# Performance work log

Measured on AMD Instinct MI355X. Metric: run time of the kernel, lower is better.

The kernel has to match this reference:

```python
import jax, jax.numpy as jnp
import numpy as np

N, E, D, L, R = 100000, 500000, 128, 2, 10
EPS = 1e-5  # BatchNorm1d default eps


def setup_inputs() -> dict:
    key = jax.random.key(0)
    ks = jax.random.split(key, 10)
    return {
        "in_node_emb": jax.random.normal(ks[0], (N, D), jnp.float32),
        "in_rel_emb": jax.random.normal(ks[1], (R, D), jnp.float32),
        "w_in": jax.random.normal(ks[2], (L, D, D), jnp.float32) * 0.05,
        "w_out": jax.random.normal(ks[3], (L, D, D), jnp.float32) * 0.05,
        "w_loop": jax.random.normal(ks[4], (L, D, D), jnp.float32) * 0.05,
        "w_rel": jax.random.normal(ks[5], (L, D, D), jnp.float32) * 0.05,
        "loop_rel": jax.random.normal(ks[6], (L, 1, D), jnp.float32) * 0.05,
        "bias": jnp.zeros((L, D), jnp.float32),
        "edge_src": jax.random.randint(ks[7], (E,), 0, N),
        "edge_dst": jax.random.randint(ks[8], (E,), 0, N),
        "edge_type": jax.random.randint(ks[9], (E,), 0, R),
    }


def _gcn_forward(in_node_emb, in_rel_emb, w_in, w_out, w_loop, w_rel, loop_rel,
                 bias, edge_src, edge_dst, edge_type):
    x, r = in_node_emb, in_rel_emb
    ones_e = jnp.ones((E,), in_node_emb.dtype)
    for l in range(L):
        rel = jnp.concatenate([r, loop_rel[l]], axis=0)  # [R+1, D]; last row = self-loop relation
        rel_e = rel[edge_type]                            # [E, D] per-edge relation embedding

        def directed_msg(row, col, w):
            # gather -> compose ('mult') -> linear -> degree norm -> scatter-add at row
            comp = x[col] * rel_e                         # [E, D]
            m = comp @ w                                  # [E, D]
            deg = jnp.zeros((N,), x.dtype).at[row].add(ones_e)
            dinv = jnp.where(deg > 0, jax.lax.rsqrt(deg), 0.0)
            m = m * (dinv[row] * dinv[col])[:, None]
            return jnp.zeros((N, D), x.dtype).at[row].add(m)

        in_res = directed_msg(edge_src, edge_dst, w_in[l])   # original direction (src<-dst msgs)
        out_res = directed_msg(edge_dst, edge_src, w_out[l]) # mirrored direction
        loop_res = (x * loop_rel[l]) @ w_loop[l]             # self-loop (no norm)
        out = (in_res + out_res + loop_res) * (1.0 / 3.0) + bias[l]
        # BatchNorm1d over nodes, batch statistics, gamma=1 beta=0
        mean = out.mean(axis=0)
        var = out.var(axis=0)
        out = (out - mean) * jax.lax.rsqrt(var + EPS)
        x = jnp.tanh(out)
        r = (rel @ w_rel[l])[:-1]                            # transform rels, drop loop row
    return x, r


def reference(in_node_emb, in_rel_emb, w_in, w_out, w_loop, w_rel, loop_rel,
              bias, edge_src, edge_dst, edge_type):
    return _gcn_forward(in_node_emb, in_rel_emb, w_in, w_out, w_loop, w_rel,
                        loop_rel, bias, edge_src, edge_dst, edge_type)
```

## Files before the change

kernel.cpp:

```cpp
#include <hip/hip_runtime.h>
#include <math.h>

#define Nn 100000
#define Ee 500000
#define Dd 128
#define Rr 10
#define ND (Nn * Dd)
#define SCAN_CHUNK 1024
#define NBLK ((Nn + SCAN_CHUNK - 1) / SCAN_CHUNK)
#define LDK 136
#define EPSF 1e-5f
#define XBLK (ND / 8 / 256)

typedef _Float16 half_t;
typedef __attribute__((ext_vector_type(2))) _Float16 h2;
typedef __attribute__((ext_vector_type(8))) _Float16 half8;
typedef __attribute__((ext_vector_type(4))) float f32x4;
typedef unsigned short ushort;
typedef unsigned int uint;
typedef unsigned long long u64;

union H8 { uint4 q; _Float16 h[8]; h2 p[4]; };

__device__ __forceinline__ void atomAddF(float* p, float v) {
    unsafeAtomicAdd(p, v);
}

__global__ void kzeroi(int* p, int n) {
    int i = blockIdx.x * blockDim.x + threadIdx.x;
    int stride = gridDim.x * blockDim.x;
    for (; i < n; i += stride) p[i] = 0;
}

__global__ void khist(const int* __restrict__ src, const int* __restrict__ dst,
                      int* cnt_s, int* cnt_d, int ne) {
    int e = blockIdx.x * blockDim.x + threadIdx.x;
    if (e < ne) {
        atomicAdd(&cnt_s[src[e]], 1);
        atomicAdd(&cnt_d[dst[e]], 1);
    }
}

__global__ __launch_bounds__(256) void kscan1(
    const int* __restrict__ cnt_s, const int* __restrict__ cnt_d,
    int* off_s, int* off_d, int* bsum_s, int* bsum_d,
    float* dinv_s, float* dinv_d) {
    int dir = blockIdx.x >= NBLK;
    int lb = blockIdx.x - dir * NBLK;
    const int* cnt = dir ? cnt_d : cnt_s;
    int* off = dir ? off_d : off_s;
    int* bsum = dir ? bsum_d : bsum_s;
    float* dinv = dir ? dinv_d : dinv_s;
    __shared__ int s[256];
    int tid = threadIdx.x;
    int base = lb * SCAN_CHUNK + tid * 4;
    int v[4], sum = 0;
#pragma unroll
    for (int q = 0; q < 4; q++) {
        int c = (base + q < Nn) ? cnt[base + q] : 0;
        v[q] = c;
        sum += c;
        if (base + q < Nn) dinv[base + q] = (c > 0) ? rsqrtf((float)c) : 0.f;
    }
    s[tid] = sum;
    __syncthreads();
#pragma unroll
    for (int ofs = 1; ofs < 256; ofs <<= 1) {
        int t = (tid >= ofs) ? s[tid - ofs] : 0;
        __syncthreads();
        s[tid] += t;
        __syncthreads();
    }
    if (tid == 255) bsum[lb] = s[255];
    int run = s[tid] - sum;
#pragma unroll
    for (int q = 0; q < 4; q++) {
        if (base + q < Nn) off[base + q] = run;
        run += v[q];
    }
}

__global__ __launch_bounds__(128) void kscan2(int* bsum_s, int* bsum_d,
                                              int* off_s, int* off_d) {
    int dir = blockIdx.x;
    int* bsum = dir ? bsum_d : bsum_s;
    int* off = dir ? off_d : off_s;
    __shared__ int s[128];
    int tid = threadIdx.x;
    int v = (tid < NBLK) ? bsum[tid] : 0;
    s[tid] = v;
    __syncthreads();
#pragma unroll
    for (int ofs = 1; ofs < 128; ofs <<= 1) {
        int t = (tid >= ofs) ? s[tid - ofs] : 0;
        __syncthreads();
        s[tid] += t;
        __syncthreads();
    }
    if (tid < NBLK) bsum[tid] = s[tid] - v;
    if (tid == 127) off[Nn] = s[127];
}

__global__ void kscan3(int* off_s, int* off_d, const int* __restrict__ bsum_s,
                       const int* __restrict__ bsum_d, int* cur_s, int* cur_d) {
    int idx = blockIdx.x * blockDim.x + threadIdx.x;
    if (idx >= 2 * Nn) return;
    int dir = idx >= Nn;
    int i = idx - dir * Nn;
    int* off = dir ? off_d : off_s;
    const int* bsum = dir ? bsum_d : bsum_s;
    int* cur = dir ? cur_d : cur_s;
    int o = off[i] + bsum[i >> 10];
    off[i] = o;
    cur[i] = o;
}

__global__ void kscatter(const int* __restrict__ src, const int* __restrict__ dst,
                         const int* __restrict__ typ,
                         const float* __restrict__ dinv_s, const float* __restrict__ dinv_d,
                         int* cur_s, int* cur_d,
                         u64* rec_s, u64* rec_d, int ne) {
    int e = blockIdx.x * blockDim.x + threadIdx.x;
    if (e >= ne) return;
    int s = src[e], d = dst[e], t = typ[e];
    int ps = atomicAdd(&cur_s[s], 1);
    rec_s[ps] = (u64)(uint)((d << 4) | t) |
                ((u64)__float_as_uint(dinv_s[s] * dinv_s[d]) << 32);
    int pd = atomicAdd(&cur_d[d], 1);
    rec_d[pd] = (u64)(uint)((s << 4) | t) |
                ((u64)__float_as_uint(dinv_d[d] * dinv_d[s]) << 32);
}

__global__ __launch_bounds__(256) void kprep(
    const float* __restrict__ x, const float* __restrict__ lr0,
    const float* __restrict__ w_in, const float* __restrict__ w_out,
    const float* __restrict__ w_loop, const float* __restrict__ w_rel,
    const float* __restrict__ r0,
    half_t* __restrict__ xb, half_t* __restrict__ xlb,
    half_t* __restrict__ Wt, half_t* __restrict__ rel0p, half_t* __restrict__ rel1p,
    float* __restrict__ r2out) {
    int blk = blockIdx.x;
    int tid = threadIdx.x;
    if (blk < XBLK) {
        int idx = blk * 256 + tid;
        int base = idx * 8;
        int k = base & 127;
        float4 v0 = *(const float4*)(x + base);
        float4 v1 = *(const float4*)(x + base + 4);
        float4 l0 = *(const float4*)(lr0 + k);
        float4 l1 = *(const float4*)(lr0 + k + 4);
        H8 xo, xl;
        xo.h[0] = (half_t)v0.x; xo.h[1] = (half_t)v0.y; xo.h[2] = (half_t)v0.z; xo.h[3] = (half_t)v0.w;
        xo.h[4] = (half_t)v1.x; xo.h[5] = (half_t)v1.y; xo.h[6] = (half_t)v1.z; xo.h[7] = (half_t)v1.w;
        xl.h[0] = (half_t)(v0.x * l0.x); xl.h[1] = (half_t)(v0.y * l0.y);
        xl.h[2] = (half_t)(v0.z * l0.z); xl.h[3] = (half_t)(v0.w * l0.w);
        xl.h[4] = (half_t)(v1.x * l1.x); xl.h[5] = (half_t)(v1.y * l1.y);
        xl.h[6] = (half_t)(v1.z * l1.z); xl.h[7] = (half_t)(v1.w * l1.w);
        *(uint4*)(xb + base) = xo.q;
        *(uint4*)(xlb + base) = xl.q;
    } else if (blk < XBLK + 384) {
        int idx = (blk - XBLK) * 256 + tid;
        int l = idx >= 49152;
        int rem = idx - l * 49152;
        int p = rem >> 14, ri = rem & 16383;
        int n = ri >> 7, k = ri & 127;
        const float* W = (p == 0) ? (w_in + l * 16384)
                       : ((p == 1) ? (w_out + l * 16384) : (w_loop + l * 16384));
        Wt[idx] = (half_t)W[k * 128 + n];
    } else if (blk == XBLK + 384) {
        __shared__ float sr[Rr * Dd];
        for (int i = tid; i < Rr * Dd; i += 256) sr[i] = r0[i];
        __syncthreads();
        for (int ph = 0; ph < 2; ph++) {
            const float* w = w_rel + ph * 16384;
            float o[5];
#pragma unroll
            for (int q = 0; q < 5; q++) {
                int oi = tid + q * 256;
                int row = oi >> 7, j = oi & 127;
                float acc = 0.f;
                for (int k = 0; k < 128; k++) acc += sr[row * 128 + k] * w[k * 128 + j];
                o[q] = acc;
            }
            __syncthreads();
#pragma unroll
            for (int q = 0; q < 5; q++) {
                int oi = tid + q * 256;
                sr[oi] = o[q];
                if (ph == 0) rel1p[oi] = (half_t)o[q];
                else r2out[oi] = o[q];
            }
            __syncthreads();
        }
        for (int i = Rr * Dd + tid; i < 16 * Dd; i += 256) rel1p[i] = (half_t)0.f;
    } else {
        for (int i = tid; i < 16 * Dd; i += 256)
            rel0p[i] = (i < Rr * Dd) ? (half_t)r0[i] : (half_t)0.f;
    }
}

__global__ __launch_bounds__(256) void kgather(
    const int* __restrict__ off_s, const u64* __restrict__ rec_s,
    const int* __restrict__ off_d, const u64* __restrict__ rec_d,
    const half_t* __restrict__ xb, const half_t* __restrict__ relp,
    half_t* __restrict__ aggin, half_t* __restrict__ aggout, int gb) {
    __shared__ uint4 sRel[256];
    sRel[threadIdx.x] = ((const uint4*)relp)[threadIdx.x];
    __syncthreads();

    int blk = blockIdx.x;
    const int* off; const u64* rec; half_t* agg;
    if (blk < gb) { off = off_s; rec = rec_s; agg = aggin; }
    else { blk -= gb; off = off_d; rec = rec_d; agg = aggout; }
    int wv = threadIdx.x >> 6;
    int lane = threadIdx.x & 63;
    int nq = lane >> 4;
    int hl = lane & 15;
    int node = blk * 16 + wv * 4 + nq;
    bool valid = node < Nn;
    int nodec = valid ? node : (Nn - 1);
    int b = off[nodec];
    int n_it = valid ? (off[nodec + 1] - b) : 0;

    const uint4* x16 = (const uint4*)xb;
    h2 acc0 = {(half_t)0.f, (half_t)0.f}, acc1 = acc0, acc2 = acc0, acc3 = acc0;

    int it = 0;
    for (; it + 1 < n_it; it += 2) {
        u64 rr0 = rec[b + it];
        u64 rr1 = rec[b + it + 1];
        uint p0 = (uint)rr0, p1 = (uint)rr1;
        H8 xv0, xv1, rv0, rv1;
        xv0.q = x16[(size_t)(p0 >> 4) * 16 + hl];
        xv1.q = x16[(size_t)(p1 >> 4) * 16 + hl];
        rv0.q = sRel[(p0 & 15u) * 16 + hl];
        rv1.q = sRel[(p1 & 15u) * 16 + hl];
        half_t w0h = (half_t)__uint_as_float((uint)(rr0 >> 32));
        half_t w1h = (half_t)__uint_as_float((uint)(rr1 >> 32));
        h2 w0 = {w0h, w0h}, w1 = {w1h, w1h};
        acc0 += (xv0.p[0] * rv0.p[0]) * w0;
        acc1 += (xv0.p[1] * rv0.p[1]) * w0;
        acc2 += (xv0.p[2] * rv0.p[2]) * w0;
        acc3 += (xv0.p[3] * rv0.p[3]) * w0;
        acc0 += (xv1.p[0] * rv1.p[0]) * w1;
        acc1 += (xv1.p[1] * rv1.p[1]) * w1;
        acc2 += (xv1.p[2] * rv1.p[2]) * w1;
        acc3 += (xv1.p[3] * rv1.p[3]) * w1;
    }
    if (it < n_it) {
        u64 rr0 = rec[b + it];
        uint p0 = (uint)rr0;
        H8 xv0, rv0;
        xv0.q = x16[(size_t)(p0 >> 4) * 16 + hl];
        rv0.q = sRel[(p0 & 15u) * 16 + hl];
        half_t w0h = (half_t)__uint_as_float((uint)(rr0 >> 32));
        h2 w0 = {w0h, w0h};
        acc0 += (xv0.p[0] * rv0.p[0]) * w0;
        acc1 += (xv0.p[1] * rv0.p[1]) * w0;
        acc2 += (xv0.p[2] * rv0.p[2]) * w0;
        acc3 += (xv0.p[3] * rv0.p[3]) * w0;
    }
    if (valid) {
        H8 o;
        o.p[0] = acc0; o.p[1] = acc1; o.p[2] = acc2; o.p[3] = acc3;
        ((uint4*)agg)[(size_t)node * 16 + hl] = o.q;
    }
}

__global__ __launch_bounds__(256) void kmm(
    const half_t* __restrict__ aggin, const half_t* __restrict__ aggout,
    const half_t* __restrict__ xlb, const half_t* __restrict__ Wt,
    const float* __restrict__ bias, half_t* __restrict__ out,
    float* colsum, float* colsumsq) {
    __shared__ half_t sW[128 * LDK];
    const int tid = threadIdx.x;
    const int wv = tid >> 6;
    const int lane = tid & 63;
    const int col = lane & 15;
    const int quad = lane >> 4;
    const int m0 = blockIdx.x * 128;
    const int rowbase = m0 + wv * 32;

    f32x4 acc[2][8];
#pragma unroll
    for (int m = 0; m < 2; m++)
#pragma unroll
        for (int j = 0; j < 8; j++) acc[m][j] = (f32x4){0.f, 0.f, 0.f, 0.f};

    const half_t* Ap[3] = {aggin, aggout, xlb};
    int r0 = rowbase + col;
    int r1 = r0 + 16;
    int r0c = (r0 < Nn) ? r0 : (Nn - 1);
    int r1c = (r1 < Nn) ? r1 : (Nn - 1);

    for (int p = 0; p < 3; p++) {
        __syncthreads();
        {
            const half8* Wg = (const half8*)(Wt + p * 16384);
#pragma unroll
            for (int i = 0; i < 8; i++) {
                int c = tid + i * 256;
                int n = c >> 4, ko = (c & 15) * 8;
                *(half8*)(sW + n * LDK + ko) = Wg[c];
            }
        }
        __syncthreads();
        const half_t* A = Ap[p];
#pragma unroll
        for (int s = 0; s < 4; s++) {
            int ko = s * 32 + quad * 8;
            half8 va0 = *(const half8*)(A + r0c * Dd + ko);
            half8 va1 = *(const half8*)(A + r1c * Dd + ko);
#pragma unroll
            for (int j = 0; j < 8; j++) {
                half8 vb = *(const half8*)(sW + (j * 16 + col) * LDK + ko);
                acc[0][j] = __builtin_amdgcn_mfma_f32_16x16x32_f16(va0, vb, acc[0][j], 0, 0, 0);
                acc[1][j] = __builtin_amdgcn_mfma_f32_16x16x32_f16(va1, vb, acc[1][j], 0, 0, 0);
            }
        }
    }

    const float inv3 = 1.f / 3.f;
    float bcol[8], sum[8], ssq[8];
#pragma unroll
    for (int j = 0; j < 8; j++) {
        bcol[j] = bias[j * 16 + col];
        sum[j] = 0.f; ssq[j] = 0.f;
    }
#pragma unroll
    for (int m = 0; m < 2; m++) {
        int rb = rowbase + m * 16;
        if (rb < Nn) {
#pragma unroll
            for (int j = 0; j < 8; j++) {
#pragma unroll
                for (int r = 0; r < 4; r++) {
                    float v = acc[m][j][r] * inv3 + bcol[j];
                    out[(rb + quad * 4 + r) * Dd + j * 16 + col] = (half_t)v;
                    sum[j] += v;
                    ssq[j] += v * v;
                }
            }
        }
    }
#pragma unroll
    for (int j = 0; j < 8; j++) {
        sum[j] += __shfl_xor(sum[j], 16, 64);
        sum[j] += __shfl_xor(sum[j], 32, 64);
        ssq[j] += __shfl_xor(ssq[j], 16, 64);
        ssq[j] += __shfl_xor(ssq[j], 32, 64);
    }
    __syncthreads();
    float* sred = (float*)sW;
    if (quad == 0) {
#pragma unroll
        for (int j = 0; j < 8; j++) {
            sred[wv * 128 + j * 16 + col] = sum[j];
            sred[512 + wv * 128 + j * 16 + col] = ssq[j];
        }
    }
    __syncthreads();
    if (tid < 128) {
        float s = 0.f, s2 = 0.f;
#pragma unroll
        for (int w = 0; w < 4; w++) {
            s += sred[w * 128 + tid];
            s2 += sred[512 + w * 128 + tid];
        }
        atomAddF(&colsum[tid], s);
        atomAddF(&colsumsq[tid], s2);
    }
}

__global__ __launch_bounds__(256) void knorm0(const half_t* __restrict__ outh,
                                              const float* __restrict__ colsum,
                                              const float* __restrict__ colsumsq,
                                              const float* __restrict__ lr,
                                              half_t* __restrict__ xb,
                                              half_t* __restrict__ xlb) {
    __shared__ float sm[128], srs[128];
    int tid = threadIdx.x;
    if (tid < 128) {
        float m = colsum[tid] * (1.f / (float)Nn);
        float v = colsumsq[tid] * (1.f / (float)Nn) - m * m;
        sm[tid] = m;
        srs[tid] = rsqrtf(v + EPSF);
    }
    __syncthreads();
    int idx = blockIdx.x * 256 + tid;
    int base = idx * 8;
    int k = base & 127;
    H8 v; v.q = *(const uint4*)(outh + base);
    H8 xo, xl;
#pragma unroll
    for (int q = 0; q < 8; q++) {
        float t = tanhf(((float)v.h[q] - sm[k + q]) * srs[k + q]);
        xo.h[q] = (half_t)t;
        xl.h[q] = (half_t)(t * lr[k + q]);
    }
    *(uint4*)(xb + base) = xo.q;
    *(uint4*)(xlb + base) = xl.q;
}

__global__ __launch_bounds__(256) void knorm1(const half_t* __restrict__ outh,
                                              const float* __restrict__ colsum,
                                              const float* __restrict__ colsumsq,
                                              float* __restrict__ xn) {
    __shared__ float sm[128], srs[128];
    int tid = threadIdx.x;
    if (tid < 128) {
        float m = colsum[tid] * (1.f / (float)Nn);
        float v = colsumsq[tid] * (1.f / (float)Nn) - m * m;
        sm[tid] = m;
        srs[tid] = rsqrtf(v + EPSF);
    }
    __syncthreads();
    int idx = blockIdx.x * 256 + tid;
    int base = idx * 8;
    int k = base & 127;
    H8 v; v.q = *(const uint4*)(outh + base);
    float4 o0, o1;
    o0.x = tanhf(((float)v.h[0] - sm[k + 0]) * srs[k + 0]);
    o0.y = tanhf(((float)v.h[1] - sm[k + 1]) * srs[k + 1]);
    o0.z = tanhf(((float)v.h[2] - sm[k + 2]) * srs[k + 2]);
    o0.w = tanhf(((float)v.h[3] - sm[k + 3]) * srs[k + 3]);
    o1.x = tanhf(((float)v.h[4] - sm[k + 4]) * srs[k + 4]);
    o1.y = tanhf(((float)v.h[5] - sm[k + 5]) * srs[k + 5]);
    o1.z = tanhf(((float)v.h[6] - sm[k + 6]) * srs[k + 6]);
    o1.w = tanhf(((float)v.h[7] - sm[k + 7]) * srs[k + 7]);
    *(float4*)(xn + base) = o0;
    *(float4*)(xn + base + 4) = o1;
}

extern "C" void kernel_launch(void* const* d_in, const int* in_sizes, int n_in,
                              void* d_out, int out_size, void* d_ws, size_t ws_size,
                              hipStream_t stream) {
    const float* x0      = (const float*)d_in[0];
    const float* r0      = (const float*)d_in[1];
    const float* w_in    = (const float*)d_in[2];
    const float* w_out   = (const float*)d_in[3];
    const float* w_loop  = (const float*)d_in[4];
    const float* w_rel   = (const float*)d_in[5];
    const float* looprel = (const float*)d_in[6];
    const float* bias    = (const float*)d_in[7];
    const int* esrc = (const int*)d_in[8];
    const int* edst = (const int*)d_in[9];
    const int* etyp = (const int*)d_in[10];
    float* outp = (float*)d_out;

    half_t* us = (half_t*)d_ws;
    half_t* aggin_h  = us;
    half_t* aggout_h = us + (size_t)ND;
    half_t* xb       = us + 2 * (size_t)ND;
    half_t* xlb      = us + 3 * (size_t)ND;
    half_t* outh     = us + 4 * (size_t)ND;
    half_t* Wt       = us + 5 * (size_t)ND;
    half_t* rel0p    = Wt + 2 * 49152;
    half_t* rel1p    = rel0p + 16 * Dd;
    u64* rec_s = (u64*)(rel1p + 16 * Dd);
    u64* rec_d = rec_s + (Ee + 64);
    float* fp = (float*)(rec_d + (Ee + 64));
    float* dinv_s  = fp;   fp += Nn;
    float* dinv_d  = fp;   fp += Nn;
    int* ip = (int*)fp;
    int* cnt_s  = ip;  ip += Nn;
    int* cnt_d  = ip;  ip += Nn;
    float* colsumA = (float*)ip;  ip += 2 * Dd;
    float* colsumB = (float*)ip;  ip += 2 * Dd;
    int* off_s  = ip;  ip += Nn + 1;
    int* off_d  = ip;  ip += Nn + 1;
    int* cur_s  = ip;  ip += Nn;
    int* cur_d  = ip;  ip += Nn;
    int* bsum_s = ip;  ip += 128;
    int* bsum_d = ip;  ip += 128;

    kzeroi<<<256, 256, 0, stream>>>(cnt_s, 2 * Nn + 4 * Dd);
    khist<<<(Ee + 255) / 256, 256, 0, stream>>>(esrc, edst, cnt_s, cnt_d, Ee);
    kscan1<<<2 * NBLK, 256, 0, stream>>>(cnt_s, cnt_d, off_s, off_d, bsum_s, bsum_d,
                                         dinv_s, dinv_d);
    kscan2<<<2, 128, 0, stream>>>(bsum_s, bsum_d, off_s, off_d);
    kscan3<<<(2 * Nn + 255) / 256, 256, 0, stream>>>(off_s, off_d, bsum_s, bsum_d,
                                                     cur_s, cur_d);
    kscatter<<<(Ee + 255) / 256, 256, 0, stream>>>(esrc, edst, etyp, dinv_s, dinv_d,
                                                   cur_s, cur_d, rec_s, rec_d, Ee);
    kprep<<<XBLK + 384 + 2, 256, 0, stream>>>(
        x0, looprel, w_in, w_out, w_loop, w_rel, r0,
        xb, xlb, Wt, rel0p, rel1p, outp + (size_t)ND);

    const int gb = (Nn + 15) / 16;
    for (int l = 0; l < 2; l++) {
        const half_t* relp = l ? rel1p : rel0p;
        float* cs = l ? colsumB : colsumA;
        kgather<<<2 * gb, 256, 0, stream>>>(off_s, rec_s, off_d, rec_d,
                                            xb, relp, aggin_h, aggout_h, gb);
        kmm<<<(Nn + 127) / 128, 256, 0, stream>>>(aggin_h, aggout_h, xlb, Wt + l * 49152,
                                                  bias + l * Dd, outh, cs, cs + Dd);
        if (l == 0) {
            knorm0<<<ND / 8 / 256, 256, 0, stream>>>(outh, cs, cs + Dd, looprel + Dd, xb, xlb);
        } else {
            knorm1<<<ND / 8 / 256, 256, 0, stream>>>(outh, cs, cs + Dd, outp);
        }
    }
}
```

Baseline: 448.3 us.

## Fuse CSR build kernels and defer block-prefix add to consumers

Merges the edge histogram with the fp16 conversion of x, and merges the edge scatter with weight transpose and relation prep. This cuts the setup launch count. kscan3 is dropped: the per-block scan offsets (bsum) are added lazily, in the scatter when positions are computed and in the gather when edge ranges are read. Edge processing is vectorized to four edges per thread with int4 loads. The cost is extra bsum lookups in the gather and scatter, and fewer threads per edge batch, which can limit latency hiding on the atomics.

```diff
diff --git a/kernel.cpp b/kernel.cpp
--- a/kernel.cpp
+++ b/kernel.cpp
@@ -11,6 +11,7 @@
 #define LDK 136
 #define EPSF 1e-5f
 #define XBLK (ND / 8 / 256)
+#define EPTB ((Ee / 4 + 255) / 256)
 
 typedef _Float16 half_t;
 typedef __attribute__((ext_vector_type(2))) _Float16 h2;
@@ -32,117 +33,28 @@
     for (; i < n; i += stride) p[i] = 0;
 }
 
-__global__ void khist(const int* __restrict__ src, const int* __restrict__ dst,
-                      int* cnt_s, int* cnt_d, int ne) {
-    int e = blockIdx.x * blockDim.x + threadIdx.x;
-    if (e < ne) {
-        atomicAdd(&cnt_s[src[e]], 1);
-        atomicAdd(&cnt_d[dst[e]], 1);
-    }
-}
-
-__global__ __launch_bounds__(256) void kscan1(
-    const int* __restrict__ cnt_s, const int* __restrict__ cnt_d,
-    int* off_s, int* off_d, int* bsum_s, int* bsum_d,
-    float* dinv_s, float* dinv_d) {
-    int dir = blockIdx.x >= NBLK;
-    int lb = blockIdx.x - dir * NBLK;
-    const int* cnt = dir ? cnt_d : cnt_s;
-    int* off = dir ? off_d : off_s;
-    int* bsum = dir ? bsum_d : bsum_s;
-    float* dinv = dir ? dinv_d : dinv_s;
-    __shared__ int s[256];
-    int tid = threadIdx.x;
-    int base = lb * SCAN_CHUNK + tid * 4;
-    int v[4], sum = 0;
-#pragma unroll
-    for (int q = 0; q < 4; q++) {
-        int c = (base + q < Nn) ? cnt[base + q] : 0;
-        v[q] = c;
-        sum += c;
-        if (base + q < Nn) dinv[base + q] = (c > 0) ? rsqrtf((float)c) : 0.f;
-    }
-    s[tid] = sum;
-    __syncthreads();
-#pragma unroll
-    for (int ofs = 1; ofs < 256; ofs <<= 1) {
-        int t = (tid >= ofs) ? s[tid - ofs] : 0;
-        __syncthreads();
-        s[tid] += t;
-        __syncthreads();
-    }
-    if (tid == 255) bsum[lb] = s[255];
-    int run = s[tid] - sum;
-#pragma unroll
-    for (int q = 0; q < 4; q++) {
-        if (base + q < Nn) off[base + q] = run;
-        run += v[q];
-    }
-}
-
-__global__ __launch_bounds__(128) void kscan2(int* bsum_s, int* bsum_d,
-                                              int* off_s, int* off_d) {
-    int dir = blockIdx.x;
-    int* bsum = dir ? bsum_d : bsum_s;
-    int* off = dir ? off_d : off_s;
-    __shared__ int s[128];
-    int tid = threadIdx.x;
-    int v = (tid < NBLK) ? bsum[tid] : 0;
-    s[tid] = v;
-    __syncthreads();
-#pragma unroll
-    for (int ofs = 1; ofs < 128; ofs <<= 1) {
-        int t = (tid >= ofs) ? s[tid - ofs] : 0;
-        __syncthreads();
-        s[tid] += t;
-        __syncthreads();
-    }
-    if (tid < NBLK) bsum[tid] = s[tid] - v;
-    if (tid == 127) off[Nn] = s[127];
-}
-
-__global__ void kscan3(int* off_s, int* off_d, const int* __restrict__ bsum_s,
-                       const int* __restrict__ bsum_d, int* cur_s, int* cur_d) {
-    int idx = blockIdx.x * blockDim.x + threadIdx.x;
-    if (idx >= 2 * Nn) return;
-    int dir = idx >= Nn;
-    int i = idx - dir * Nn;
-    int* off = dir ? off_d : off_s;
-    const int* bsum = dir ? bsum_d : bsum_s;
-    int* cur = dir ? cur_d : cur_s;
-    int o = off[i] + bsum[i >> 10];
-    off[i] = o;
-    cur[i] = o;
-}
-
-__global__ void kscatter(const int* __restrict__ src, const int* __restrict__ dst,
-                         const int* __restrict__ typ,
-                         const float* __restrict__ dinv_s, const float* __restrict__ dinv_d,
-                         int* cur_s, int* cur_d,
-                         u64* rec_s, u64* rec_d, int ne) {
-    int e = blockIdx.x * blockDim.x + threadIdx.x;
-    if (e >= ne) return;
-    int s = src[e], d = dst[e], t = typ[e];
-    int ps = atomicAdd(&cur_s[s], 1);
-    rec_s[ps] = (u64)(uint)((d << 4) | t) |
-                ((u64)__float_as_uint(dinv_s[s] * dinv_s[d]) << 32);
-    int pd = atomicAdd(&cur_d[d], 1);
-    rec_d[pd] = (u64)(uint)((s << 4) | t) |
-                ((u64)__float_as_uint(dinv_d[d] * dinv_d[s]) << 32);
-}
-
-__global__ __launch_bounds__(256) void kprep(
+__global__ __launch_bounds__(256) void khistprep(
+    const int* __restrict__ src, const int* __restrict__ dst,
+    int* cnt_s, int* cnt_d,
     const float* __restrict__ x, const float* __restrict__ lr0,
-    const float* __restrict__ w_in, const float* __restrict__ w_out,
-    const float* __restrict__ w_loop, const float* __restrict__ w_rel,
-    const float* __restrict__ r0,
-    half_t* __restrict__ xb, half_t* __restrict__ xlb,
-    half_t* __restrict__ Wt, half_t* __restrict__ rel0p, half_t* __restrict__ rel1p,
-    float* __restrict__ r2out) {
+    half_t* __restrict__ xb, half_t* __restrict__ xlb) {
     int blk = blockIdx.x;
     int tid = threadIdx.x;
-    if (blk < XBLK) {
-        int idx = blk * 256 + tid;
+    if (blk < EPTB) {
+        int e4 = (blk * 256 + tid) * 4;
+        if (e4 >= Ee) return;
+        int4 s4 = *(const int4*)(src + e4);
+        int4 d4 = *(const int4*)(dst + e4);
+        atomicAdd(&cnt_s[s4.x], 1);
+        atomicAdd(&cnt_s[s4.y], 1);
+        atomicAdd(&cnt_s[s4.z], 1);
+        atomicAdd(&cnt_s[s4.w], 1);
+        atomicAdd(&cnt_d[d4.x], 1);
+        atomicAdd(&cnt_d[d4.y], 1);
+        atomicAdd(&cnt_d[d4.z], 1);
+        atomicAdd(&cnt_d[d4.w], 1);
+    } else {
+        int idx = (blk - EPTB) * 256 + tid;
         int base = idx * 8;
         int k = base & 127;
         float4 v0 = *(const float4*)(x + base);
@@ -158,8 +70,116 @@
         xl.h[6] = (half_t)(v1.z * l1.z); xl.h[7] = (half_t)(v1.w * l1.w);
         *(uint4*)(xb + base) = xo.q;
         *(uint4*)(xlb + base) = xl.q;
-    } else if (blk < XBLK + 384) {
-        int idx = (blk - XBLK) * 256 + tid;
+    }
+}
+
+__global__ __launch_bounds__(256) void kscan1(
+    const int* __restrict__ cnt_s, const int* __restrict__ cnt_d,
+    int* off_s, int* off_d, int* bsum_s, int* bsum_d,
+    float* dinv_s, float* dinv_d, int* cur_s, int* cur_d) {
+    int dir = blockIdx.x >= NBLK;
+    int lb = blockIdx.x - dir * NBLK;
+    const int* cnt = dir ? cnt_d : cnt_s;
+    int* off = dir ? off_d : off_s;
+    int* bsum = dir ? bsum_d : bsum_s;
+    float* dinv = dir ? dinv_d : dinv_s;
+    int* cur = dir ? cur_d : cur_s;
+    __shared__ int s[256];
+    int tid = threadIdx.x;
+    int base = lb * SCAN_CHUNK + tid * 4;
+    int v[4], sum = 0;
+#pragma unroll
+    for (int q = 0; q < 4; q++) {
+        int c = (base + q < Nn) ? cnt[base + q] : 0;
+        v[q] = c;
+        sum += c;
+        if (base + q < Nn) dinv[base + q] = (c > 0) ? rsqrtf((float)c) : 0.f;
+    }
+    s[tid] = sum;
+    __syncthreads();
+#pragma unroll
+    for (int ofs = 1; ofs < 256; ofs <<= 1) {
+        int t = (tid >= ofs) ? s[tid - ofs] : 0;
+        __syncthreads();
+        s[tid] += t;
+        __syncthreads();
+    }
+    if (tid == 255) {
+        bsum[lb] = s[255];
+        if (lb == NBLK - 1) off[Nn] = s[255];
+    }
+    int run = s[tid] - sum;
+#pragma unroll
+    for (int q = 0; q < 4; q++) {
+        if (base + q < Nn) { off[base + q] = run; cur[base + q] = run; }
+        run += v[q];
+    }
+}
+
+__global__ __launch_bounds__(128) void kscan2(int* bsum_s, int* bsum_d) {
+    int dir = blockIdx.x;
+    int* bsum = dir ? bsum_d : bsum_s;
+    __shared__ int s[128];
+    int tid = threadIdx.x;
+    int v = (tid < NBLK) ? bsum[tid] : 0;
+    s[tid] = v;
+    __syncthreads();
+#pragma unroll
+    for (int ofs = 1; ofs < 128; ofs <<= 1) {
+        int t = (tid >= ofs) ? s[tid - ofs] : 0;
+        __syncthreads();
+        s[tid] += t;
+        __syncthreads();
+    }
+    if (tid < NBLK) bsum[tid] = s[tid] - v;
+}
+
+__global__ __launch_bounds__(256) void kscatprep(
+    const int* __restrict__ src, const int* __restrict__ dst,
+    const int* __restrict__ typ,
+    const float* __restrict__ dinv_s, const float* __restrict__ dinv_d,
+    int* cur_s, int* cur_d,
+    const int* __restrict__ bsum_s, const int* __restrict__ bsum_d,
+    u64* rec_s, u64* rec_d,
+    const float* __restrict__ w_in, const float* __restrict__ w_out,
+    const float* __restrict__ w_loop, const float* __restrict__ w_rel,
+    const float* __restrict__ r0,
+    half_t* __restrict__ Wt, half_t* __restrict__ rel0p, half_t* __restrict__ rel1p,
+    float* __restrict__ r2out) {
+    int blk = blockIdx.x;
+    int tid = threadIdx.x;
+    if (blk < EPTB) {
+        int e4 = (blk * 256 + tid) * 4;
+        if (e4 >= Ee) return;
+        int4 s4 = *(const int4*)(src + e4);
+        int4 d4 = *(const int4*)(dst + e4);
+        int4 t4 = *(const int4*)(typ + e4);
+        int ss[4] = {s4.x, s4.y, s4.z, s4.w};
+        int dd[4] = {d4.x, d4.y, d4.z, d4.w};
+        int tt[4] = {t4.x, t4.y, t4.z, t4.w};
+        float vs_s[4], vs_d[4], vd_d[4], vd_s[4];
+#pragma unroll
+        for (int q = 0; q < 4; q++) {
+            vs_s[q] = dinv_s[ss[q]];
+            vs_d[q] = dinv_s[dd[q]];
+            vd_d[q] = dinv_d[dd[q]];
+            vd_s[q] = dinv_d[ss[q]];
+        }
+        int ps[4], pd[4];
+#pragma unroll
+        for (int q = 0; q < 4; q++) {
+            ps[q] = atomicAdd(&cur_s[ss[q]], 1) + bsum_s[ss[q] >> 10];
+            pd[q] = atomicAdd(&cur_d[dd[q]], 1) + bsum_d[dd[q] >> 10];
+        }
+#pragma unroll
+        for (int q = 0; q < 4; q++) {
+            rec_s[ps[q]] = (u64)(uint)((dd[q] << 4) | tt[q]) |
+                           ((u64)__float_as_uint(vs_s[q] * vs_d[q]) << 32);
+            rec_d[pd[q]] = (u64)(uint)((ss[q] << 4) | tt[q]) |
+                           ((u64)__float_as_uint(vd_d[q] * vd_s[q]) << 32);
+        }
+    } else if (blk < EPTB + 384) {
+        int idx = (blk - EPTB) * 256 + tid;
         int l = idx >= 49152;
         int rem = idx - l * 49152;
         int p = rem >> 14, ri = rem & 16383;
@@ -167,7 +187,7 @@
         const float* W = (p == 0) ? (w_in + l * 16384)
                        : ((p == 1) ? (w_out + l * 16384) : (w_loop + l * 16384));
         Wt[idx] = (half_t)W[k * 128 + n];
-    } else if (blk == XBLK + 384) {
+    } else if (blk == EPTB + 384) {
         __shared__ float sr[Rr * Dd];
         for (int i = tid; i < Rr * Dd; i += 256) sr[i] = r0[i];
         __syncthreads();
@@ -202,6 +222,7 @@
 __global__ __launch_bounds__(256) void kgather(
     const int* __restrict__ off_s, const u64* __restrict__ rec_s,
     const int* __restrict__ off_d, const u64* __restrict__ rec_d,
+    const int* __restrict__ bsum_s, const int* __restrict__ bsum_d,
     const half_t* __restrict__ xb, const half_t* __restrict__ relp,
     half_t* __restrict__ aggin, half_t* __restrict__ aggout, int gb) {
     __shared__ uint4 sRel[256];
@@ -209,9 +230,9 @@
     __syncthreads();
 
     int blk = blockIdx.x;
-    const int* off; const u64* rec; half_t* agg;
-    if (blk < gb) { off = off_s; rec = rec_s; agg = aggin; }
-    else { blk -= gb; off = off_d; rec = rec_d; agg = aggout; }
+    const int* off; const u64* rec; half_t* agg; const int* bsum;
+    if (blk < gb) { off = off_s; rec = rec_s; agg = aggin; bsum = bsum_s; }
+    else { blk -= gb; off = off_d; rec = rec_d; agg = aggout; bsum = bsum_d; }
     int wv = threadIdx.x >> 6;
     int lane = threadIdx.x & 63;
     int nq = lane >> 4;
@@ -219,8 +240,9 @@
     int node = blk * 16 + wv * 4 + nq;
     bool valid = node < Nn;
     int nodec = valid ? node : (Nn - 1);
-    int b = off[nodec];
-    int n_it = valid ? (off[nodec + 1] - b) : 0;
+    int b = off[nodec] + bsum[nodec >> 10];
+    int e = off[nodec + 1] + bsum[(nodec + 1) >> 10];
+    int n_it = valid ? (e - b) : 0;
 
     const uint4* x16 = (const uint4*)xb;
     h2 acc0 = {(half_t)0.f, (half_t)0.f}, acc1 = acc0, acc2 = acc0, acc3 = acc0;
@@ -475,23 +497,21 @@
     int* bsum_d = ip;  ip += 128;
 
     kzeroi<<<256, 256, 0, stream>>>(cnt_s, 2 * Nn + 4 * Dd);
-    khist<<<(Ee + 255) / 256, 256, 0, stream>>>(esrc, edst, cnt_s, cnt_d, Ee);
+    khistprep<<<EPTB + XBLK, 256, 0, stream>>>(esrc, edst, cnt_s, cnt_d,
+                                               x0, looprel, xb, xlb);
     kscan1<<<2 * NBLK, 256, 0, stream>>>(cnt_s, cnt_d, off_s, off_d, bsum_s, bsum_d,
-                                         dinv_s, dinv_d);
-    kscan2<<<2, 128, 0, stream>>>(bsum_s, bsum_d, off_s, off_d);
-    kscan3<<<(2 * Nn + 255) / 256, 256, 0, stream>>>(off_s, off_d, bsum_s, bsum_d,
-                                                     cur_s, cur_d);
-    kscatter<<<(Ee + 255) / 256, 256, 0, stream>>>(esrc, edst, etyp, dinv_s, dinv_d,
-                                                   cur_s, cur_d, rec_s, rec_d, Ee);
-    kprep<<<XBLK + 384 + 2, 256, 0, stream>>>(
-        x0, looprel, w_in, w_out, w_loop, w_rel, r0,
-        xb, xlb, Wt, rel0p, rel1p, outp + (size_t)ND);
+                                         dinv_s, dinv_d, cur_s, cur_d);
+    kscan2<<<2, 128, 0, stream>>>(bsum_s, bsum_d);
+    kscatprep<<<EPTB + 384 + 2, 256, 0, stream>>>(
+        esrc, edst, etyp, dinv_s, dinv_d, cur_s, cur_d, bsum_s, bsum_d,
+        rec_s, rec_d, w_in, w_out, w_loop, w_rel, r0,
+        Wt, rel0p, rel1p, outp + (size_t)ND);
 
     const int gb = (Nn + 15) / 16;
     for (int l = 0; l < 2; l++) {
         const half_t* relp = l ? rel1p : rel0p;
         float* cs = l ? colsumB : colsumA;
-        kgather<<<2 * gb, 256, 0, stream>>>(off_s, rec_s, off_d, rec_d,
+        kgather<<<2 * gb, 256, 0, stream>>>(off_s, rec_s, off_d, rec_d, bsum_s, bsum_d,
                                             xb, relp, aggin_h, aggout_h, gb);
         kmm<<<(Nn + 127) / 128, 256, 0, stream>>>(aggin_h, aggout_h, xlb, Wt + l * 49152,
                                                   bias + l * Dd, outh, cs, cs + Dd);
```

Result: no change. 446.8 us (-0.3%).
